# Optimization experiments

Measured on AMD Instinct MI355X. Metric: run time of the kernel, lower is better.

## Reference

```python
import jax, jax.numpy as jnp
import numpy as np

WEIGHT = 1e-9
SIGMA_RGB = 15.0
SIGMA_XY = 100.0
SCALE = 0.5  # downscale factor (integer stride 2)


def _down_nearest(x):
    # PyTorch F.interpolate(mode='nearest', scale_factor=0.5): out[i]=in[2i]
    return x[..., ::2, ::2]


def _down_bilinear2(x):
    # PyTorch bilinear, align_corners=False, scale 0.5: src = 2i + 0.5
    # -> average of the 2x2 input block (exact, no antialiasing).
    N, K, H, W = x.shape
    return x.reshape(N, K, H // 2, 2, W // 2, 2).mean(axis=(3, 5))


def setup_inputs() -> dict:
    key = jax.random.key(0)
    k1, k2, k3 = jax.random.split(key, 3)
    N, K, H, W = 8, 21, 128, 128
    images = jax.random.uniform(k1, (N, 3, H, W), jnp.float32) * 255.0
    logS = jax.random.normal(k2, (N, K, H, W), jnp.float32)
    log1_S = jax.random.normal(k3, (N, K, H, W), jnp.float32)
    ROIs = jnp.ones((N, H, W), jnp.float32)
    return {"images": images, "logS": logS, "log1_S": log1_S, "ROIs": ROIs}


def reference(images, logS, log1_S, ROIs):
    # 1) downscale all inputs (scale_factor = 0.5)
    img = _down_nearest(images)            # [N,3,h,w]
    lS = _down_bilinear2(logS)             # [N,K,h,w]
    l1S = _down_bilinear2(log1_S)          # [N,K,h,w]
    roi = _down_nearest(ROIs)              # [N,h,w]

    N, K, h, w = lS.shape
    P = h * w
    sxy = SIGMA_XY * SCALE

    # bilateral features: (r,g,b)/sigma_rgb ++ (x,y)/sigma_xy
    yy, xx = jnp.meshgrid(jnp.arange(h, dtype=jnp.float32),
                          jnp.arange(w, dtype=jnp.float32), indexing='ij')
    feat_pos = jnp.stack([xx, yy], axis=-1).reshape(P, 2) / sxy          # [P,2]
    feat_rgb = (img / SIGMA_RGB).transpose(0, 2, 3, 1).reshape(N, P, 3)  # [N,P,3]
    feats = jnp.concatenate(
        [feat_rgb, jnp.broadcast_to(feat_pos, (N, P, 2))], axis=-1)      # [N,P,5]

    # ROI masking (applied to both logS and log(1-S), as in the torch code)
    roi_f = roi.reshape(N, 1, P)
    lS_m = lS.reshape(N, K, P) * roi_f
    l1S_m = l1S.reshape(N, K, P) * roi_f

    def per_image(f, a, b):
        # dense Gaussian bilateral kernel W_pq = exp(-0.5 ||f_p - f_q||^2)
        sq = jnp.sum(f * f, axis=-1)                      # [P]
        d2 = sq[:, None] + sq[None, :] - 2.0 * (f @ f.T)  # [P,P]
        Wk = jnp.exp(-0.5 * d2)
        Ab = jnp.einsum('pq,kq->kp', Wk, b)               # W @ log(1-S)
        return jnp.sum(a * Ab)                            # logS . (W log(1-S))

    losses = jax.vmap(per_image)(feats, lS_m, l1S_m)      # [N]
    return WEIGHT * jnp.sum(losses) / N
```

## Files before the change

### kernel.cpp

```cpp
#include <hip/hip_runtime.h>

#define NIMG 8
#define KCH 21
#define HW2 16384
#define PD 4096
#define NT 256
#define RT 4
#define SQRT_LOG2E 1.2011224087864498f

typedef __attribute__((ext_vector_type(8))) short short8;
typedef __attribute__((ext_vector_type(4))) float f32x4;

__device__ __forceinline__ unsigned short bf16rne(float x) {
    unsigned u = __float_as_uint(x);
    unsigned r = (u + 0x7FFFu + ((u >> 16) & 1u)) >> 16;
    return (unsigned short)r;
}
__device__ __forceinline__ float bf2f(unsigned short b) {
    return __uint_as_float(((unsigned)b) << 16);
}

__global__ __launch_bounds__(256)
void prep_kernel(const float* __restrict__ images,
                 const float* __restrict__ logS, const float* __restrict__ log1S,
                 const float* __restrict__ rois,
                 unsigned short* __restrict__ AopM, unsigned short* __restrict__ BopM,
                 unsigned short* __restrict__ GA, unsigned short* __restrict__ GB)
{
    const int bid = blockIdx.x;
    if (bid < 2048) {
        unsigned t = bid * 256 + threadIdx.x;
        int h = t & 2047;
        int k = (t >> 11) & 31;
        int n = t >> 16;
        int p0 = h << 1;
        size_t o = (size_t)((n * NT + (p0 >> 4)) * 4 + (k >> 3)) * 128
                 + (p0 & 15) * 8 + (k & 7);
        unsigned short a0 = 0, a1 = 0, b0 = 0, b1 = 0;
        if (k < KCH) {
            int i = p0 >> 6, j0 = p0 & 63;
            int base = (i << 8) + (j0 << 1);
            int nk = n * KCH + k;
            const float* ls = logS  + (size_t)nk * HW2;
            const float* l1 = log1S + (size_t)nk * HW2;
            float4 lsa = *reinterpret_cast<const float4*>(ls + base);
            float4 lsb = *reinterpret_cast<const float4*>(ls + base + 128);
            float4 l1a = *reinterpret_cast<const float4*>(l1 + base);
            float4 l1b = *reinterpret_cast<const float4*>(l1 + base + 128);
            float4 rr  = *reinterpret_cast<const float4*>(rois + (size_t)n * HW2 + base);
            a0 = bf16rne(0.25f * (lsa.x + lsa.y + lsb.x + lsb.y) * rr.x);
            a1 = bf16rne(0.25f * (lsa.z + lsa.w + lsb.z + lsb.w) * rr.z);
            b0 = bf16rne(0.25f * (l1a.x + l1a.y + l1b.x + l1b.y) * rr.x);
            b1 = bf16rne(0.25f * (l1a.z + l1a.w + l1b.z + l1b.w) * rr.z);
        }
        AopM[o] = a0; AopM[o + 8] = a1;
        BopM[o] = b0; BopM[o + 8] = b1;
    } else {
        int t = (bid - 2048) * 256 + threadIdx.x;
        int n = t >> 12, p = t & 4095;
        int i = p >> 6, j = p & 63;
        int base = (i << 8) + (j << 1);
        const float* img = images + (size_t)n * 3 * HW2;

        float f[5];
        f[0] = img[base]           * (SQRT_LOG2E / 15.0f);
        f[1] = img[HW2 + base]     * (SQRT_LOG2E / 15.0f);
        f[2] = img[2 * HW2 + base] * (SQRT_LOG2E / 15.0f);
        f[3] = (float)j * (SQRT_LOG2E / 50.0f);
        f[4] = (float)i * (SQRT_LOG2E / 50.0f);

        unsigned short hi[5], lo[5];
        float hsum = 0.0f;
#pragma unroll
        for (int c = 0; c < 5; ++c) {
            hi[c] = bf16rne(f[c]);
            float hf = bf2f(hi[c]);
            lo[c] = bf16rne(f[c] - hf);
            float fh = hf + bf2f(lo[c]);
            hsum = fmaf(fh, fh, hsum);
        }
        float nh = -0.5f * hsum;
        unsigned short nhh = bf16rne(nh);
        unsigned short nhl = bf16rne(nh - bf2f(nhh));
        const unsigned short one = 0x3F80;

        unsigned short av[32], bv[32];
#pragma unroll
        for (int s = 0; s < 32; ++s) { av[s] = 0; bv[s] = 0; }
#pragma unroll
        for (int c = 0; c < 5; ++c) {
            av[c]      = hi[c]; bv[c]      = hi[c];
            av[c + 5]  = hi[c]; bv[c + 5]  = lo[c];
            av[c + 10] = lo[c]; bv[c + 10] = hi[c];
            av[c + 15] = lo[c]; bv[c + 15] = lo[c];
        }
        av[20] = nhh; bv[20] = one;
        av[21] = nhl; bv[21] = one;
        av[22] = one; bv[22] = nhh;
        av[23] = one; bv[23] = nhl;

        int rt = p >> 4, m = p & 15;
        unsigned short* ga = GA + (size_t)(n * NT + rt) * 512 + m * 8;
        unsigned short* gb = GB + (size_t)(n * NT + rt) * 512 + m * 8;
#pragma unroll
        for (int g = 0; g < 4; ++g)
#pragma unroll
            for (int e2 = 0; e2 < 4; ++e2) {
                int s = g * 8 + e2 * 2;
                ushort2 pa; pa.x = av[s]; pa.y = av[s + 1];
                ushort2 pb; pb.x = bv[s]; pb.y = bv[s + 1];
                *reinterpret_cast<ushort2*>(ga + g * 128 + e2 * 2) = pa;
                *reinterpret_cast<ushort2*>(gb + g * 128 + e2 * 2) = pb;
            }
    }
}

__global__ __launch_bounds__(256)
void crf_kernel(const unsigned short* __restrict__ AopM,
                const unsigned short* __restrict__ BopM,
                const unsigned short* __restrict__ GA,
                const unsigned short* __restrict__ GB,
                float* __restrict__ partials)
{
    const int tid = threadIdx.x;
    const int l = tid & 63;
    const int w = __builtin_amdgcn_readfirstlane(tid >> 6);
    const int unit = blockIdx.x * 4 + w;
    const int n = unit >> 9;
    const int rem = unit & 511;
    const int rt0 = (rem >> 3) << 2;
    const int seg = rem & 7;
    const int lf = l * 8;

    short8 aM[RT], aG[RT];
#pragma unroll
    for (int i = 0; i < RT; ++i) {
        const size_t tb = (size_t)(n * NT + rt0 + i) * 512;
        aM[i] = *reinterpret_cast<const short8*>(AopM + tb + lf);
        aG[i] = *reinterpret_cast<const short8*>(GA   + tb + lf);
    }

    const int ct0 = seg * 32;
    const unsigned short* bMb = BopM + (size_t)(n * NT + ct0) * 512;
    const unsigned short* bGb = GB   + (size_t)(n * NT + ct0) * 512;

    const f32x4 zero = {0.0f, 0.0f, 0.0f, 0.0f};
    float acc[RT] = {0.0f, 0.0f, 0.0f, 0.0f};

    short8 bm = *reinterpret_cast<const short8*>(bMb + lf);
    short8 bg = *reinterpret_cast<const short8*>(bGb + lf);

#pragma unroll 4
    for (int tt = 0; tt < 32; ++tt) {
        const int nx = (tt + 1 < 32) ? tt + 1 : 31;
        short8 bm_n = *reinterpret_cast<const short8*>(bMb + nx * 512 + lf);
        short8 bg_n = *reinterpret_cast<const short8*>(bGb + nx * 512 + lf);

#pragma unroll
        for (int i = 0; i < RT; ++i) {
            f32x4 mm = __builtin_amdgcn_mfma_f32_16x16x32_bf16(aM[i], bm, zero, 0, 0, 0);
            f32x4 gg = __builtin_amdgcn_mfma_f32_16x16x32_bf16(aG[i], bg, zero, 0, 0, 0);
#pragma unroll
            for (int r = 0; r < 4; ++r) {
                float wgt;
                asm("v_exp_f32 %0, %1" : "=v"(wgt) : "v"(gg[r]));
                acc[i] = fmaf(wgt, mm[r], acc[i]);
            }
        }
        bm = bm_n; bg = bg_n;
    }

    float partial = (acc[0] + acc[1]) + (acc[2] + acc[3]);
#pragma unroll
    for (int off = 32; off; off >>= 1)
        partial += __shfl_down(partial, off, 64);

    __shared__ float sred[4];
    if (l == 0) sred[w] = partial;
    __syncthreads();
    if (tid == 0)
        partials[blockIdx.x] = (sred[0] + sred[1]) + (sred[2] + sred[3]);
}

__global__ __launch_bounds__(256)
void reduce_kernel(const float* __restrict__ partials, float* __restrict__ out, int count)
{
    __shared__ float s[256];
    float sum = 0.0f;
    for (int i = threadIdx.x; i < count; i += 256) sum += partials[i];
    s[threadIdx.x] = sum;
    __syncthreads();
    for (int st = 128; st > 0; st >>= 1) {
        if (threadIdx.x < st) s[threadIdx.x] += s[threadIdx.x + st];
        __syncthreads();
    }
    if (threadIdx.x == 0) out[0] = s[0] * (1e-9f / 8.0f);
}

extern "C" void kernel_launch(void* const* d_in, const int* in_sizes, int n_in,
                              void* d_out, int out_size, void* d_ws, size_t ws_size,
                              hipStream_t stream)
{
    const float* images = (const float*)d_in[0];
    const float* logS   = (const float*)d_in[1];
    const float* log1S  = (const float*)d_in[2];
    const float* rois   = (const float*)d_in[3];
    float* out = (float*)d_out;

    unsigned short* AopM = (unsigned short*)d_ws;
    unsigned short* BopM = AopM + (1u << 20);
    unsigned short* GA   = BopM + (1u << 20);
    unsigned short* GB   = GA   + (1u << 20);
    float* partials      = (float*)(GB + (1u << 20));

    prep_kernel<<<2176, 256, 0, stream>>>(images, logS, log1S, rois,
                                          AopM, BopM, GA, GB);
    crf_kernel<<<1024, 256, 0, stream>>>(AopM, BopM, GA, GB, partials);
    reduce_kernel<<<1, 256, 0, stream>>>(partials, out, 1024);
}
```

Baseline: 109.8 us.

## Widen CRF row tiles to 8 and fold the final reduction into atomics

Each wave now holds 8 row tiles of A operands in registers and sweeps 16 column tiles instead of 4 rows by 32 columns. This doubles reuse of each loaded B fragment and halves the B-operand traffic per unit of MFMA work. The separate reduce kernel is removed: each block atomically adds its scaled partial into the output, which the prep kernel zeroes first. This saves one launch but makes the floating-point summation order nondeterministic and raises register pressure.

```diff
diff --git a/kernel.cpp b/kernel.cpp
--- a/kernel.cpp
+++ b/kernel.cpp
@@ -5,7 +5,8 @@
 #define HW2 16384
 #define PD 4096
 #define NT 256
-#define RT 4
+#define RT 8
+#define NSEG 16
 #define SQRT_LOG2E 1.2011224087864498f
 
 typedef __attribute__((ext_vector_type(8))) short short8;
@@ -25,9 +26,11 @@
                  const float* __restrict__ logS, const float* __restrict__ log1S,
                  const float* __restrict__ rois,
                  unsigned short* __restrict__ AopM, unsigned short* __restrict__ BopM,
-                 unsigned short* __restrict__ GA, unsigned short* __restrict__ GB)
+                 unsigned short* __restrict__ GA, unsigned short* __restrict__ GB,
+                 float* __restrict__ out)
 {
     const int bid = blockIdx.x;
+    if (bid == 0 && threadIdx.x == 0) out[0] = 0.0f;
     if (bid < 2048) {
         unsigned t = bid * 256 + threadIdx.x;
         int h = t & 2047;
@@ -120,7 +123,7 @@
                 const unsigned short* __restrict__ BopM,
                 const unsigned short* __restrict__ GA,
                 const unsigned short* __restrict__ GB,
-                float* __restrict__ partials)
+                float* __restrict__ out)
 {
     const int tid = threadIdx.x;
     const int l = tid & 63;
@@ -128,8 +131,8 @@
     const int unit = blockIdx.x * 4 + w;
     const int n = unit >> 9;
     const int rem = unit & 511;
-    const int rt0 = (rem >> 3) << 2;
-    const int seg = rem & 7;
+    const int rt0 = (rem >> 4) << 3;
+    const int seg = rem & 15;
     const int lf = l * 8;
 
     short8 aM[RT], aG[RT];
@@ -140,19 +143,19 @@
         aG[i] = *reinterpret_cast<const short8*>(GA   + tb + lf);
     }
 
-    const int ct0 = seg * 32;
+    const int ct0 = seg * 16;
     const unsigned short* bMb = BopM + (size_t)(n * NT + ct0) * 512;
     const unsigned short* bGb = GB   + (size_t)(n * NT + ct0) * 512;
 
     const f32x4 zero = {0.0f, 0.0f, 0.0f, 0.0f};
-    float acc[RT] = {0.0f, 0.0f, 0.0f, 0.0f};
+    float acc[RT] = {};
 
     short8 bm = *reinterpret_cast<const short8*>(bMb + lf);
     short8 bg = *reinterpret_cast<const short8*>(bGb + lf);
 
 #pragma unroll 4
-    for (int tt = 0; tt < 32; ++tt) {
-        const int nx = (tt + 1 < 32) ? tt + 1 : 31;
+    for (int tt = 0; tt < 16; ++tt) {
+        const int nx = (tt + 1 < 16) ? tt + 1 : 15;
         short8 bm_n = *reinterpret_cast<const short8*>(bMb + nx * 512 + lf);
         short8 bg_n = *reinterpret_cast<const short8*>(bGb + nx * 512 + lf);
 
@@ -170,7 +173,8 @@
         bm = bm_n; bg = bg_n;
     }
 
-    float partial = (acc[0] + acc[1]) + (acc[2] + acc[3]);
+    float partial = ((acc[0] + acc[1]) + (acc[2] + acc[3]))
+                  + ((acc[4] + acc[5]) + (acc[6] + acc[7]));
 #pragma unroll
     for (int off = 32; off; off >>= 1)
         partial += __shfl_down(partial, off, 64);
@@ -178,23 +182,10 @@
     __shared__ float sred[4];
     if (l == 0) sred[w] = partial;
     __syncthreads();
-    if (tid == 0)
-        partials[blockIdx.x] = (sred[0] + sred[1]) + (sred[2] + sred[3]);
-}
-
-__global__ __launch_bounds__(256)
-void reduce_kernel(const float* __restrict__ partials, float* __restrict__ out, int count)
-{
-    __shared__ float s[256];
-    float sum = 0.0f;
-    for (int i = threadIdx.x; i < count; i += 256) sum += partials[i];
-    s[threadIdx.x] = sum;
-    __syncthreads();
-    for (int st = 128; st > 0; st >>= 1) {
-        if (threadIdx.x < st) s[threadIdx.x] += s[threadIdx.x + st];
-        __syncthreads();
-    }
-    if (threadIdx.x == 0) out[0] = s[0] * (1e-9f / 8.0f);
+    if (tid == 0) {
+        float s = (sred[0] + sred[1]) + (sred[2] + sred[3]);
+        atomicAdd(out, s * (1e-9f / 8.0f));
+    }
 }
 
 extern "C" void kernel_launch(void* const* d_in, const int* in_sizes, int n_in,
@@ -211,10 +202,8 @@
     unsigned short* BopM = AopM + (1u << 20);
     unsigned short* GA   = BopM + (1u << 20);
     unsigned short* GB   = GA   + (1u << 20);
-    float* partials      = (float*)(GB + (1u << 20));
 
     prep_kernel<<<2176, 256, 0, stream>>>(images, logS, log1S, rois,
-                                          AopM, BopM, GA, GB);
-    crf_kernel<<<1024, 256, 0, stream>>>(AopM, BopM, GA, GB, partials);
-    reduce_kernel<<<1, 256, 0, stream>>>(partials, out, 1024);
-}
+                                          AopM, BopM, GA, GB, out);
+    crf_kernel<<<1024, 256, 0, stream>>>(AopM, BopM, GA, GB, out);
+}
```

Measured after the change: 110.1 us (median of 2 runs). No clear change (+0.3%).
